# Kernel tuning notes

Measured on AMD Instinct MI355X. Metric: run time of the kernel, lower is better.

## Reference

```python
import jax, jax.numpy as jnp
import numpy as np
from jax.scipy.special import erf, erfc

B, D, C = 256, 512, 85742

def setup_inputs() -> dict:
    key = jax.random.key(0)
    k1, k2, k3, k4, k5 = jax.random.split(key, 5)
    x = jax.random.normal(k1, (B, D), dtype=jnp.float32)
    mu = jax.random.normal(k2, (B, D), dtype=jnp.float32)
    std = jax.random.uniform(k3, (B, D), dtype=jnp.float32)
    weight = jax.random.normal(k4, (C, D), dtype=jnp.float32)
    label = jax.random.randint(k5, (B,), 0, C, dtype=jnp.int64)
    return {"x": x, "mu": mu, "std": std, "weight": weight, "label": label}


def reference(x, mu, std, weight, label):
    # one_hot: [B, C] float, as in F.one_hot(...).float()
    one_hot = jax.nn.one_hot(label, weight.shape[0], dtype=jnp.float32)
    # wy = one_hot @ weight (embedding gather expressed as GEMM), wi = (1 - one_hot) @ weight
    wy = one_hot @ weight                 # [B, D]
    wi = (1.0 - one_hot) @ weight         # [B, D]
    sqrt2 = jnp.sqrt(jnp.float32(2.0))
    # torch.dist(a, b) is the scalar Frobenius (L2) distance
    dist_y = jnp.abs(jnp.sqrt(jnp.sum((wy - mu) ** 2)))
    dist_i = jnp.abs(jnp.sqrt(jnp.sum((wi - mu) ** 2)))
    erf_value = erf(dist_y / (sqrt2 * std))    # [B, D] via broadcast of scalar dist
    erfc_value = erfc(dist_i / (sqrt2 * std))  # [B, D]
    loss = erf_value.sum() + erfc_value.sum()
    return loss
```

## Files before the change

### kernel.cpp

```cpp
#include <hip/hip_runtime.h>
#include <math.h>

#define DDIM 512
#define BDIM 256
#define NCLS 85742
#define NB1 2048
#define CHUNK1 ((NCLS + NB1 - 1) / NB1)

typedef float f32x4 __attribute__((ext_vector_type(4)));
#define NTL(p) __builtin_nontemporal_load(p)

__device__ __forceinline__ float wave_reduce(float v) {
    #pragma unroll
    for (int off = 32; off > 0; off >>= 1)
        v += __shfl_down(v, off, 64);
    return v;
}

__device__ __forceinline__ float block_reduce(float v, float* smem) {
    const int lane = threadIdx.x & 63;
    const int wid  = threadIdx.x >> 6;
    v = wave_reduce(v);
    if (lane == 0) smem[wid] = v;
    __syncthreads();
    if (wid == 0) {
        v = (lane < (int)(blockDim.x >> 6)) ? smem[lane] : 0.0f;
        v = wave_reduce(v);
    }
    return v;
}

__global__ __launch_bounds__(256, 4)
void colsum_partial(const float* __restrict__ W, f32x4* __restrict__ partialT,
                    float* __restrict__ sums, float* __restrict__ out) {
    const int t = threadIdx.x;
    if (blockIdx.x == 0) {
        if (t < 2) sums[t] = 0.0f;
        if (t == 2) *out = 0.0f;
    }
    const int q = t & 127;
    const int rsub = t >> 7;
    const int b = blockIdx.x;
    const f32x4* __restrict__ W4 = reinterpret_cast<const f32x4*>(W) + q;

    const int r0 = b * CHUNK1;
    const int r1 = (r0 + CHUNK1 < NCLS) ? (r0 + CHUNK1) : NCLS;

    f32x4 a0 = (f32x4)(0.f), a1 = a0, a2 = a0, a3 = a0;

    if (r1 - r0 == CHUNK1) {
        const f32x4* base = W4 + (size_t)(r0 + rsub) * 128;
        f32x4 c0 = NTL(base);
        f32x4 c1 = NTL(base + 256);
        f32x4 c2 = NTL(base + 512);
        f32x4 c3 = NTL(base + 768);
        #pragma unroll
        for (int k = 1; k <= 4; ++k) {
            const f32x4* p = base + (size_t)k * 1024;
            a0 += c0;  c0 = NTL(p);
            a1 += c1;  c1 = NTL(p + 256);
            a2 += c2;  c2 = NTL(p + 512);
            a3 += c3;  c3 = NTL(p + 768);
        }
        f32x4 cl = NTL(base + 5120);
        a0 += c0; a1 += c1; a2 += c2; a3 += c3;
        a0 += cl;
    } else {
        for (int r = r0 + rsub; r < r1; r += 2) {
            a0 += NTL(W4 + (size_t)r * 128);
        }
    }
    a0 += a1 + a2 + a3;

    __shared__ f32x4 smem[128];
    if (rsub) smem[q] = a0;
    __syncthreads();
    if (!rsub) {
        a0 += smem[q];
        partialT[(size_t)q * NB1 + b] = a0;
    }
}

__global__ __launch_bounds__(256, 4)
void reduce_dist(const f32x4* __restrict__ partialT,
                 const float* __restrict__ mu, const float* __restrict__ W,
                 const int* __restrict__ label, float* __restrict__ sums) {
    const int q = blockIdx.x;
    const int t = threadIdx.x;
    const f32x4* __restrict__ p = partialT + (size_t)q * NB1;
    f32x4 s = (f32x4)(0.f);
    #pragma unroll
    for (int k = 0; k < NB1 / 256; ++k)
        s += p[t + k * 256];
    float sx = wave_reduce(s.x), sy = wave_reduce(s.y);
    float sz = wave_reduce(s.z), sw = wave_reduce(s.w);
    __shared__ f32x4 sm[4];
    __shared__ f32x4 csm;
    if ((t & 63) == 0) sm[t >> 6] = (f32x4)(sx, sy, sz, sw);
    __syncthreads();
    if (t == 0) csm = (sm[0] + sm[1]) + (sm[2] + sm[3]);
    __syncthreads();
    const f32x4 cs = csm;

    const f32x4 m4 = reinterpret_cast<const f32x4*>(mu)[(size_t)t * 128 + q];
    const f32x4 w4 = reinterpret_cast<const f32x4*>(W)[(size_t)label[t] * 128 + q];
    f32x4 a = w4 - m4;
    f32x4 c = cs - w4 - m4;
    float dy2 = a.x * a.x + a.y * a.y + a.z * a.z + a.w * a.w;
    float di2 = c.x * c.x + c.y * c.y + c.z * c.z + c.w * c.w;

    __shared__ float rsm[8];
    dy2 = block_reduce(dy2, rsm);
    __syncthreads();
    di2 = block_reduce(di2, rsm);
    if (t == 0) {
        atomicAdd(&sums[0], dy2);
        atomicAdd(&sums[1], di2);
    }
}

__global__ __launch_bounds__(256, 4)
void loss_kernel(const float* __restrict__ stdv,
                 const float* __restrict__ sums,
                 float* __restrict__ out) {
    __shared__ float smem[8];
    const float dy = sqrtf(sums[0]);
    const float di = sqrtf(sums[1]);
    const float inv_sqrt2 = 0.70710678118654752f;
    const int i = blockIdx.x * 256 + threadIdx.x;
    f32x4 s4 = reinterpret_cast<const f32x4*>(stdv)[i];
    float acc;
    {
        float rx = inv_sqrt2 / s4.x, ry = inv_sqrt2 / s4.y;
        float rz = inv_sqrt2 / s4.z, rw = inv_sqrt2 / s4.w;
        acc  = erff(dy * rx) + erfcf(di * rx);
        acc += erff(dy * ry) + erfcf(di * ry);
        acc += erff(dy * rz) + erfcf(di * rz);
        acc += erff(dy * rw) + erfcf(di * rw);
    }
    acc = block_reduce(acc, smem);
    if (threadIdx.x == 0) atomicAdd(out, acc);
}

extern "C" void kernel_launch(void* const* d_in, const int* in_sizes, int n_in,
                              void* d_out, int out_size, void* d_ws, size_t ws_size,
                              hipStream_t stream) {
    const float* mu    = (const float*)d_in[1];
    const float* stdv  = (const float*)d_in[2];
    const float* W     = (const float*)d_in[3];
    const int*   label = (const int*)d_in[4];
    float* out = (float*)d_out;
    float* ws  = (float*)d_ws;
    float* sums = ws;
    f32x4* partialT = (f32x4*)(ws + 1024);

    colsum_partial<<<NB1, 256, 0, stream>>>(W, partialT, sums, out);
    reduce_dist<<<128, 256, 0, stream>>>(partialT, mu, W, label, sums);
    loss_kernel<<<128, 256, 0, stream>>>(stdv, sums, out);
}
```

Measured before the change: 50.02 us.

## Expand di² algebraically and move label gather into colsum kernel

Rewrites the distance for wi as sum over rows of (cs - (w+mu))², expanded into 256·cs² - 2·cs·U + Σ|w+mu|². The per-row gather of W[label] and mu now runs inside the first kernel's first 128 blocks, which writes per-row partial sums and u = w+mu to workspace. The reduce kernel then only needs column sums of partials and of u. Nontemporal loads on W are replaced with plain loads. The expanded form can lose precision through cancellation.

```diff
diff --git a/kernel.cpp b/kernel.cpp
--- a/kernel.cpp
+++ b/kernel.cpp
@@ -8,7 +8,6 @@
 #define CHUNK1 ((NCLS + NB1 - 1) / NB1)
 
 typedef float f32x4 __attribute__((ext_vector_type(4)));
-#define NTL(p) __builtin_nontemporal_load(p)
 
 __device__ __forceinline__ float wave_reduce(float v) {
     #pragma unroll
@@ -30,17 +29,20 @@
     return v;
 }
 
+#define WS_UPART 1024
+#define WS_PART  (1024 + 256 * 128 * 4)
+
 __global__ __launch_bounds__(256, 4)
-void colsum_partial(const float* __restrict__ W, f32x4* __restrict__ partialT,
-                    float* __restrict__ sums, float* __restrict__ out) {
+void colsum_partial(const float* __restrict__ W, const float* __restrict__ mu,
+                    const int* __restrict__ label, float* __restrict__ ws,
+                    float* __restrict__ out) {
     const int t = threadIdx.x;
-    if (blockIdx.x == 0) {
-        if (t < 2) sums[t] = 0.0f;
-        if (t == 2) *out = 0.0f;
+    const int b = blockIdx.x;
+    if (b == 0 && t < 2) {
+        if (t == 0) { ws[0] = 0.0f; *out = 0.0f; }
     }
     const int q = t & 127;
     const int rsub = t >> 7;
-    const int b = blockIdx.x;
     const f32x4* __restrict__ W4 = reinterpret_cast<const f32x4*>(W) + q;
 
     const int r0 = b * CHUNK1;
@@ -50,25 +52,24 @@
 
     if (r1 - r0 == CHUNK1) {
         const f32x4* base = W4 + (size_t)(r0 + rsub) * 128;
-        f32x4 c0 = NTL(base);
-        f32x4 c1 = NTL(base + 256);
-        f32x4 c2 = NTL(base + 512);
-        f32x4 c3 = NTL(base + 768);
+        f32x4 c0 = base[0];
+        f32x4 c1 = base[256];
+        f32x4 c2 = base[512];
+        f32x4 c3 = base[768];
         #pragma unroll
         for (int k = 1; k <= 4; ++k) {
             const f32x4* p = base + (size_t)k * 1024;
-            a0 += c0;  c0 = NTL(p);
-            a1 += c1;  c1 = NTL(p + 256);
-            a2 += c2;  c2 = NTL(p + 512);
-            a3 += c3;  c3 = NTL(p + 768);
+            a0 += c0;  c0 = p[0];
+            a1 += c1;  c1 = p[256];
+            a2 += c2;  c2 = p[512];
+            a3 += c3;  c3 = p[768];
         }
-        f32x4 cl = NTL(base + 5120);
+        f32x4 cl = base[5120];
         a0 += c0; a1 += c1; a2 += c2; a3 += c3;
         a0 += cl;
     } else {
-        for (int r = r0 + rsub; r < r1; r += 2) {
-            a0 += NTL(W4 + (size_t)r * 128);
-        }
+        for (int r = r0 + rsub; r < r1; r += 2)
+            a0 += W4[(size_t)r * 128];
     }
     a0 += a1 + a2 + a3;
 
@@ -77,55 +78,79 @@
     __syncthreads();
     if (!rsub) {
         a0 += smem[q];
+        f32x4* partialT = reinterpret_cast<f32x4*>(ws + WS_PART);
         partialT[(size_t)q * NB1 + b] = a0;
+    }
+
+    if (b < 128) {
+        const int row = 2 * b + rsub;
+        const int lab = label[row];
+        const f32x4 m4 = reinterpret_cast<const f32x4*>(mu)[(size_t)row * 128 + q];
+        const f32x4 w4 = reinterpret_cast<const f32x4*>(W)[(size_t)lab * 128 + q];
+        f32x4 d = w4 - m4;
+        f32x4 u = w4 + m4;
+        reinterpret_cast<f32x4*>(ws + WS_UPART)[(size_t)row * 128 + q] = u;
+        float syp = d.x * d.x + d.y * d.y + d.z * d.z + d.w * d.w;
+        float s2p = u.x * u.x + u.y * u.y + u.z * u.z + u.w * u.w;
+        __shared__ float rsm[8];
+        __syncthreads();
+        syp = block_reduce(syp, rsm);
+        __syncthreads();
+        s2p = block_reduce(s2p, rsm);
+        if (t == 0) {
+            ws[16 + b]  = syp;
+            ws[144 + b] = s2p;
+        }
     }
 }
 
 __global__ __launch_bounds__(256, 4)
-void reduce_dist(const f32x4* __restrict__ partialT,
-                 const float* __restrict__ mu, const float* __restrict__ W,
-                 const int* __restrict__ label, float* __restrict__ sums) {
+void reduce_kernel(float* __restrict__ ws) {
     const int q = blockIdx.x;
     const int t = threadIdx.x;
-    const f32x4* __restrict__ p = partialT + (size_t)q * NB1;
+    const f32x4* __restrict__ partialT =
+        reinterpret_cast<const f32x4*>(ws + WS_PART) + (size_t)q * NB1;
     f32x4 s = (f32x4)(0.f);
     #pragma unroll
     for (int k = 0; k < NB1 / 256; ++k)
-        s += p[t + k * 256];
+        s += partialT[t + k * 256];
+    f32x4 u = reinterpret_cast<const f32x4*>(ws + WS_UPART)[(size_t)t * 128 + q];
+
     float sx = wave_reduce(s.x), sy = wave_reduce(s.y);
     float sz = wave_reduce(s.z), sw = wave_reduce(s.w);
-    __shared__ f32x4 sm[4];
-    __shared__ f32x4 csm;
-    if ((t & 63) == 0) sm[t >> 6] = (f32x4)(sx, sy, sz, sw);
+    float ux = wave_reduce(u.x), uy = wave_reduce(u.y);
+    float uz = wave_reduce(u.z), uw = wave_reduce(u.w);
+    __shared__ f32x4 sm[4], um[4];
+    if ((t & 63) == 0) {
+        sm[t >> 6] = (f32x4)(sx, sy, sz, sw);
+        um[t >> 6] = (f32x4)(ux, uy, uz, uw);
+    }
     __syncthreads();
-    if (t == 0) csm = (sm[0] + sm[1]) + (sm[2] + sm[3]);
-    __syncthreads();
-    const f32x4 cs = csm;
+    if (t == 0) {
+        f32x4 cs = (sm[0] + sm[1]) + (sm[2] + sm[3]);
+        f32x4 U  = (um[0] + um[1]) + (um[2] + um[3]);
+        f32x4 si4 = 256.0f * cs * cs - 2.0f * cs * U;
+        atomicAdd(&ws[0], si4.x + si4.y + si4.z + si4.w);
+    }
 
-    const f32x4 m4 = reinterpret_cast<const f32x4*>(mu)[(size_t)t * 128 + q];
-    const f32x4 w4 = reinterpret_cast<const f32x4*>(W)[(size_t)label[t] * 128 + q];
-    f32x4 a = w4 - m4;
-    f32x4 c = cs - w4 - m4;
-    float dy2 = a.x * a.x + a.y * a.y + a.z * a.z + a.w * a.w;
-    float di2 = c.x * c.x + c.y * c.y + c.z * c.z + c.w * c.w;
-
-    __shared__ float rsm[8];
-    dy2 = block_reduce(dy2, rsm);
-    __syncthreads();
-    di2 = block_reduce(di2, rsm);
-    if (t == 0) {
-        atomicAdd(&sums[0], dy2);
-        atomicAdd(&sums[1], di2);
+    if (q == 0) {
+        __syncthreads();
+        __shared__ float rsm[8];
+        float syp = (t < 128) ? ws[16 + t]  : 0.0f;
+        float s2p = (t < 128) ? ws[144 + t] : 0.0f;
+        syp = block_reduce(syp, rsm);
+        __syncthreads();
+        s2p = block_reduce(s2p, rsm);
+        if (t == 0) { ws[1] = syp; ws[2] = s2p; }
     }
 }
 
 __global__ __launch_bounds__(256, 4)
-void loss_kernel(const float* __restrict__ stdv,
-                 const float* __restrict__ sums,
+void loss_kernel(const float* __restrict__ stdv, const float* __restrict__ ws,
                  float* __restrict__ out) {
     __shared__ float smem[8];
-    const float dy = sqrtf(sums[0]);
-    const float di = sqrtf(sums[1]);
+    const float dy = sqrtf(ws[1]);
+    const float di = sqrtf(ws[0] + ws[2]);
     const float inv_sqrt2 = 0.70710678118654752f;
     const int i = blockIdx.x * 256 + threadIdx.x;
     f32x4 s4 = reinterpret_cast<const f32x4*>(stdv)[i];
@@ -151,10 +176,8 @@
     const int*   label = (const int*)d_in[4];
     float* out = (float*)d_out;
     float* ws  = (float*)d_ws;
-    float* sums = ws;
-    f32x4* partialT = (f32x4*)(ws + 1024);
 
-    colsum_partial<<<NB1, 256, 0, stream>>>(W, partialT, sums, out);
-    reduce_dist<<<128, 256, 0, stream>>>(partialT, mu, W, label, sums);
-    loss_kernel<<<128, 256, 0, stream>>>(stdv, sums, out);
+    colsum_partial<<<NB1, 256, 0, stream>>>(W, mu, label, ws, out);
+    reduce_kernel<<<128, 256, 0, stream>>>(ws);
+    loss_kernel<<<128, 256, 0, stream>>>(stdv, ws, out);
 }
```

Measured after the change: 43.43 us. 13.2% less time.
